# Optimization experiments

Hardware: AMD Instinct MI355X
Metric: run time of the kernel (lower is better)

## Reference

```python
import jax, jax.numpy as jnp
import numpy as np

N_OBS, N_DIM, N_FUNCTIONS, N_APPLICATIONS = 65536, 256, 16, 8


def setup_inputs() -> dict:
    key = jax.random.key(0)
    k1, k2, k3, k4 = jax.random.split(key, 4)
    x = jax.random.normal(k1, (N_OBS, N_DIM), dtype=jnp.float32)
    function_indices = jax.random.randint(k2, (N_OBS, N_APPLICATIONS), 0, N_FUNCTIONS, dtype=jnp.int32)
    # Stacked Dense weights/biases, one per IFS function. Scale keeps column
    # norms well under the MaxNorm(0.99) constraint (contractive maps).
    W = jax.random.normal(k3, (N_FUNCTIONS, N_DIM, N_DIM), dtype=jnp.float32) * 0.05
    b = jax.random.normal(k4, (N_FUNCTIONS, N_DIM), dtype=jnp.float32) * 0.05
    return {"x": x, "function_indices": function_indices, "W": W, "b": b}


def reference(x, function_indices, W, b):
    # One IFS application step: compute all n_functions affine maps for every
    # point (as the original layer does), then select the per-point function.
    def step(carry, idx):
        # carry: (n_obs, n_dim); idx: (n_obs,) int
        y_all = jnp.einsum('od,fde->ofe', carry, W) + b  # (n_obs, n_funcs, n_dim)
        y = jnp.take_along_axis(y_all, idx[:, None, None].astype(jnp.int32), axis=1)[:, 0, :]
        return y, None
    # scan over the n_applications axis (leading axis after transpose)
    out, _ = jax.lax.scan(step, x, function_indices.T)
    return out
```

## Files before the change

kernel.cpp:

```cpp
#include <hip/hip_runtime.h>
#include <hip/hip_bf16.h>
#include <stdint.h>

#define N_OBS 65536
#define N_DIM 256
#define N_FUN 16
#define N_APP 8
#define MT 64
#define PERM_STRIDE (N_OBS + N_FUN * MT)
#define MAX_TILES (PERM_STRIDE / MT)
#define N_BLK 256

typedef __attribute__((ext_vector_type(8))) short v8s;
typedef __attribute__((ext_vector_type(4))) short v4s;
typedef __attribute__((ext_vector_type(4))) float v4f;

__device__ __forceinline__ unsigned short f2bf(float f) {
  union { float f; uint32_t u; } v;
  v.f = f;
  uint32_t u = v.u;
  return (unsigned short)((u + 0x7FFFu + ((u >> 16) & 1u)) >> 16);
}

__global__ void k_init(int* __restrict__ perm) {
  int tid = blockIdx.x * 256 + threadIdx.x;
  if (tid < N_APP * PERM_STRIDE) perm[tid] = -1;
}

__global__ void k_prep_w(const float* __restrict__ W, unsigned short* __restrict__ Wt) {
  int tid = blockIdx.x * 256 + threadIdx.x;
  int f = tid >> 16;
  int n = (tid >> 8) & 255;
  int k = tid & 255;
  Wt[tid] = f2bf(W[(f << 16) | (k << 8) | n]);
}

__global__ void k_hist2(const int* __restrict__ fidx, int* __restrict__ blockCnt) {
  __shared__ int h[N_APP * N_FUN];
  int tid = threadIdx.x;
  if (tid < N_APP * N_FUN) h[tid] = 0;
  __syncthreads();
  int o = blockIdx.x * 256 + tid;
  const int4* p = (const int4*)(fidx + o * N_APP);
  int4 a = p[0], b = p[1];
  atomicAdd(&h[0 * N_FUN + a.x], 1);
  atomicAdd(&h[1 * N_FUN + a.y], 1);
  atomicAdd(&h[2 * N_FUN + a.z], 1);
  atomicAdd(&h[3 * N_FUN + a.w], 1);
  atomicAdd(&h[4 * N_FUN + b.x], 1);
  atomicAdd(&h[5 * N_FUN + b.y], 1);
  atomicAdd(&h[6 * N_FUN + b.z], 1);
  atomicAdd(&h[7 * N_FUN + b.w], 1);
  __syncthreads();
  if (tid < N_APP * N_FUN) blockCnt[tid * N_BLK + blockIdx.x] = h[tid];
}

__global__ void k_scan2(const int* __restrict__ blockCnt, int* __restrict__ pb,
                        int* __restrict__ tilef, int* __restrict__ blockOff) {
  __shared__ int tot[N_APP * N_FUN];
  int i = threadIdx.x;
  if (i < N_APP * N_FUN) {
    int s = 0;
    for (int b = 0; b < N_BLK; ++b) s += blockCnt[i * N_BLK + b];
    tot[i] = s;
  }
  __syncthreads();
  if (i < N_APP) {
    int base = 0;
    for (int f = 0; f < N_FUN; ++f) {
      pb[i * 17 + f] = base;
      int c = tot[i * N_FUN + f];
      int padded = (c + MT - 1) & ~(MT - 1);
      int q0 = base / MT, q1 = (base + padded) / MT;
      for (int q = q0; q < q1; ++q) tilef[i * MAX_TILES + q] = f;
      base += padded;
    }
    pb[i * 17 + 16] = base;
  }
  __syncthreads();
  if (i < N_APP * N_FUN) {
    int t = i >> 4, f = i & 15;
    int off = pb[t * 17 + f];
    for (int b = 0; b < N_BLK; ++b) {
      blockOff[i * N_BLK + b] = off;
      off += blockCnt[i * N_BLK + b];
    }
  }
}

__global__ void k_scatter2(const int* __restrict__ fidx, const int* __restrict__ blockOff,
                           int* __restrict__ perm) {
  __shared__ int cur[N_APP * N_FUN];
  int tid = threadIdx.x;
  if (tid < N_APP * N_FUN) cur[tid] = blockOff[tid * N_BLK + blockIdx.x];
  __syncthreads();
  int o = blockIdx.x * 256 + tid;
  const int4* p = (const int4*)(fidx + o * N_APP);
  int4 a = p[0], b = p[1];
  int fs[8] = {a.x, a.y, a.z, a.w, b.x, b.y, b.z, b.w};
  #pragma unroll
  for (int t = 0; t < N_APP; ++t) {
    int pos = atomicAdd(&cur[t * N_FUN + fs[t]], 1);
    perm[t * PERM_STRIDE + pos] = o;
  }
}

__global__ void k_pos(const int* __restrict__ perm, int* __restrict__ pos) {
  int tid = blockIdx.x * 256 + threadIdx.x;
  if (tid >= 7 * PERM_STRIDE) return;
  int t = tid / PERM_STRIDE + 1;
  int s = tid - (t - 1) * PERM_STRIDE;
  int o = perm[t * PERM_STRIDE + s];
  if (o >= 0) pos[(t - 1) * N_OBS + o] = s;
}

__global__ void k_outpos(int* __restrict__ perm, const int* __restrict__ pos,
                         int* __restrict__ outpos0) {
  int tid = blockIdx.x * 256 + threadIdx.x;
  if (tid >= 7 * PERM_STRIDE) return;
  int t = tid / PERM_STRIDE;
  int s = tid - t * PERM_STRIDE;
  int o = perm[t * PERM_STRIDE + s];
  int val = (o >= 0) ? pos[t * N_OBS + o] : -1;
  if (t == 0) outpos0[s] = val;
  else perm[t * PERM_STRIDE + s] = val;
}

template <int SRC_F32, int DST_F32>
__global__ __launch_bounds__(256, 4)
void k_step(const void* __restrict__ src_, void* __restrict__ dst_,
            const unsigned short* __restrict__ Wt, const float* __restrict__ bias,
            const int* __restrict__ pb_t, const int* __restrict__ tilef_t,
            const int* __restrict__ outpos_t, const int* __restrict__ perm0) {
  __shared__ unsigned short As[MT * N_DIM];
  __shared__ int ops[MT];
  int tile = blockIdx.x;
  if (tile * MT >= pb_t[16]) return;
  int f = tilef_t[tile];
  int tid = threadIdx.x;

  if (tid < MT) ops[tid] = outpos_t[tile * MT + tid];

  if (SRC_F32) {
    const int* permBase = perm0 + tile * MT;
    #pragma unroll
    for (int i = 0; i < 8; ++i) {
      int g = tid + i * 256;
      int row = g >> 5, c = g & 31;
      int grow = permBase[row];
      if (grow < 0) grow = 0;
      const v4f* s = (const v4f*)((const float*)src_ + ((size_t)grow << 8) + (c << 3));
      v4f v0 = s[0], v1 = s[1];
      v8s val;
      val[0] = (short)f2bf(v0[0]); val[1] = (short)f2bf(v0[1]);
      val[2] = (short)f2bf(v0[2]); val[3] = (short)f2bf(v0[3]);
      val[4] = (short)f2bf(v1[0]); val[5] = (short)f2bf(v1[1]);
      val[6] = (short)f2bf(v1[2]); val[7] = (short)f2bf(v1[3]);
      *(v8s*)((char*)As + (row << 9) + ((c ^ (row & 7)) << 4)) = val;
    }
  } else {
    const unsigned short* srcT = (const unsigned short*)src_ + (size_t)tile * MT * N_DIM;
    #pragma unroll
    for (int i = 0; i < 8; ++i) {
      int g = tid + i * 256;
      int row = g >> 5, c = g & 31;
      v8s val = *(const v8s*)(srcT + (size_t)g * 8);
      *(v8s*)((char*)As + (row << 9) + ((c ^ (row & 7)) << 4)) = val;
    }
  }
  __syncthreads();

  int lane = tid & 63, wave = tid >> 6;
  int l15 = lane & 15, lq = lane >> 4;
  v4f acc[4][4] = {};
  const unsigned short* Wf = Wt + ((size_t)f << 16);

  #pragma unroll
  for (int kk = 0; kk < 8; ++kk) {
    v8s a[4];
    #pragma unroll
    for (int mt = 0; mt < 4; ++mt) {
      int row = mt * 16 + l15;
      int byte = (row << 9) + ((((kk << 2) + lq) ^ (row & 7)) << 4);
      a[mt] = *(const v8s*)((const char*)As + byte);
    }
    #pragma unroll
    for (int nt = 0; nt < 4; ++nt) {
      int n = wave * 64 + nt * 16 + l15;
      v8s bfr = *(const v8s*)(Wf + n * N_DIM + (kk << 5) + (lq << 3));
      #pragma unroll
      for (int mt = 0; mt < 4; ++mt)
        acc[mt][nt] = __builtin_amdgcn_mfma_f32_16x16x32_bf16(bfr, a[mt], acc[mt][nt], 0, 0, 0);
    }
  }

  const float* bf_ = bias + f * N_DIM;
  if (DST_F32) {
    float* dout = (float*)dst_;
    #pragma unroll
    for (int mt = 0; mt < 4; ++mt) {
      int m = mt * 16 + l15;
      int orow = ops[m];
      if (orow >= 0) {
        #pragma unroll
        for (int nt = 0; nt < 4; ++nt) {
          int n0 = wave * 64 + nt * 16 + lq * 4;
          v4f bv = *(const v4f*)(bf_ + n0);
          v4f o = acc[mt][nt] + bv;
          *(v4f*)(dout + ((size_t)orow << 8) + n0) = o;
        }
      }
    }
  } else {
    __syncthreads();
    #pragma unroll
    for (int mt = 0; mt < 4; ++mt) {
      int m = mt * 16 + l15;
      #pragma unroll
      for (int nt = 0; nt < 4; ++nt) {
        int n0 = wave * 64 + nt * 16 + lq * 4;
        v4f bv = *(const v4f*)(bf_ + n0);
        v4s pk;
        pk[0] = (short)f2bf(acc[mt][nt][0] + bv[0]);
        pk[1] = (short)f2bf(acc[mt][nt][1] + bv[1]);
        pk[2] = (short)f2bf(acc[mt][nt][2] + bv[2]);
        pk[3] = (short)f2bf(acc[mt][nt][3] + bv[3]);
        int c = n0 >> 3;
        *(v4s*)((char*)As + (m << 9) + ((c ^ (m & 7)) << 4) + ((n0 & 7) << 1)) = pk;
      }
    }
    __syncthreads();
    unsigned short* dst = (unsigned short*)dst_;
    #pragma unroll
    for (int i = 0; i < 8; ++i) {
      int g = tid + i * 256;
      int row = g >> 5, c = g & 31;
      int op = ops[row];
      if (op >= 0) {
        v8s v = *(const v8s*)((char*)As + (row << 9) + ((c ^ (row & 7)) << 4));
        *(v8s*)(dst + (size_t)op * N_DIM + c * 8) = v;
      }
    }
  }
}

extern "C" void kernel_launch(void* const* d_in, const int* in_sizes, int n_in,
                              void* d_out, int out_size, void* d_ws, size_t ws_size,
                              hipStream_t stream) {
  const float* x = (const float*)d_in[0];
  const int* fidx = (const int*)d_in[1];
  const float* W = (const float*)d_in[2];
  const float* bias = (const float*)d_in[3];

  char* ws = (char*)d_ws;
  unsigned short* carryA = (unsigned short*)ws;
  int* blockCnt = (int*)ws;
  int* blockOff = (int*)(ws + 131072);
  int* pos      = (int*)(ws + 262144);
  unsigned short* Wt = (unsigned short*)(ws + 34078720);
  int* perm    = (int*)(ws + 36175872);
  int* pb      = (int*)(ws + 38305792);
  int* tilef   = (int*)(ws + 38306336);
  int* outpos0 = (int*)(ws + 38339648);
  unsigned short* carryB = (unsigned short*)d_out;

  k_init<<<(N_APP * PERM_STRIDE + 255) / 256, 256, 0, stream>>>(perm);
  k_prep_w<<<(N_FUN * N_DIM * N_DIM) / 256, 256, 0, stream>>>(W, Wt);
  k_hist2<<<N_BLK, 256, 0, stream>>>(fidx, blockCnt);
  k_scan2<<<1, 128, 0, stream>>>(blockCnt, pb, tilef, blockOff);
  k_scatter2<<<N_BLK, 256, 0, stream>>>(fidx, blockOff, perm);
  k_pos<<<(7 * PERM_STRIDE + 255) / 256, 256, 0, stream>>>(perm, pos);
  k_outpos<<<(7 * PERM_STRIDE + 255) / 256, 256, 0, stream>>>(perm, pos, outpos0);

  k_step<1, 0><<<MAX_TILES, 256, 0, stream>>>(x, carryA, Wt, bias, pb, tilef, outpos0, perm);
  for (int t = 1; t < 7; ++t) {
    const unsigned short* s = (t & 1) ? carryA : carryB;
    unsigned short* d = (t & 1) ? carryB : carryA;
    k_step<0, 0><<<MAX_TILES, 256, 0, stream>>>(
        s, d, Wt, bias, pb + t * 17, tilef + t * MAX_TILES,
        perm + t * PERM_STRIDE, nullptr);
  }
  k_step<0, 1><<<MAX_TILES, 256, 0, stream>>>(
      carryA, d_out, Wt, bias, pb + 7 * 17, tilef + 7 * MAX_TILES,
      perm + 7 * PERM_STRIDE, nullptr);
}
```

Measured before the change: 388.1 us.

## Compose pairs of affine maps to halve the number of sequential GEMM steps

When the workspace is large enough, the code precomputes all 256 composed matrices W_f·W_g and the matching composed biases. Each point is then bucketed by its pair of consecutive function indices, so the forward pass runs 4 grouped GEMM steps instead of 8. This removes half of the per-step activation reads and writes and the launch overhead, at the cost of an extra composition GEMM and more padded tiles, since there are 256 groups instead of 16. Rounding the composed matrices to bf16 changes numerics. It also adds an XCD-aware block swizzle and raises the occupancy hint to 5.

```diff
diff --git a/kernel.cpp b/kernel.cpp
--- a/kernel.cpp
+++ b/kernel.cpp
@@ -7,8 +7,6 @@
 #define N_FUN 16
 #define N_APP 8
 #define MT 64
-#define PERM_STRIDE (N_OBS + N_FUN * MT)
-#define MAX_TILES (PERM_STRIDE / MT)
 #define N_BLK 256
 
 typedef __attribute__((ext_vector_type(8))) short v8s;
@@ -22,65 +20,73 @@
   return (unsigned short)((u + 0x7FFFu + ((u >> 16) & 1u)) >> 16);
 }
 
-__global__ void k_init(int* __restrict__ perm) {
+__device__ __forceinline__ int xcd_swz(int bid, int n) {
+  int q = n >> 3;
+  return (bid & 7) * q + (bid >> 3);
+}
+
+__global__ void k_init(int* __restrict__ perm, int total) {
   int tid = blockIdx.x * 256 + threadIdx.x;
-  if (tid < N_APP * PERM_STRIDE) perm[tid] = -1;
+  if (tid < total) perm[tid] = -1;
 }
 
 __global__ void k_prep_w(const float* __restrict__ W, unsigned short* __restrict__ Wt) {
   int tid = blockIdx.x * 256 + threadIdx.x;
-  int f = tid >> 16;
-  int n = (tid >> 8) & 255;
-  int k = tid & 255;
+  int f = tid >> 16, n = (tid >> 8) & 255, k = tid & 255;
   Wt[tid] = f2bf(W[(f << 16) | (k << 8) | n]);
 }
 
-__global__ void k_hist2(const int* __restrict__ fidx, int* __restrict__ blockCnt) {
-  __shared__ int h[N_APP * N_FUN];
+__global__ void k_hist(const int* __restrict__ fidx, int* __restrict__ blockCnt,
+                       int pairMode) {
+  __shared__ int h[1024];
+  int nb = pairMode ? 1024 : 128;
   int tid = threadIdx.x;
-  if (tid < N_APP * N_FUN) h[tid] = 0;
-  __syncthreads();
-  int o = blockIdx.x * 256 + tid;
-  const int4* p = (const int4*)(fidx + o * N_APP);
+  for (int j = tid; j < nb; j += 256) h[j] = 0;
+  __syncthreads();
+  size_t o = blockIdx.x * 256 + tid;
+  const int4* p = (const int4*)(fidx + o * 8);
   int4 a = p[0], b = p[1];
-  atomicAdd(&h[0 * N_FUN + a.x], 1);
-  atomicAdd(&h[1 * N_FUN + a.y], 1);
-  atomicAdd(&h[2 * N_FUN + a.z], 1);
-  atomicAdd(&h[3 * N_FUN + a.w], 1);
-  atomicAdd(&h[4 * N_FUN + b.x], 1);
-  atomicAdd(&h[5 * N_FUN + b.y], 1);
-  atomicAdd(&h[6 * N_FUN + b.z], 1);
-  atomicAdd(&h[7 * N_FUN + b.w], 1);
-  __syncthreads();
-  if (tid < N_APP * N_FUN) blockCnt[tid * N_BLK + blockIdx.x] = h[tid];
-}
-
-__global__ void k_scan2(const int* __restrict__ blockCnt, int* __restrict__ pb,
-                        int* __restrict__ tilef, int* __restrict__ blockOff) {
-  __shared__ int tot[N_APP * N_FUN];
+  int fs[8] = {a.x, a.y, a.z, a.w, b.x, b.y, b.z, b.w};
+  if (pairMode) {
+    #pragma unroll
+    for (int t = 0; t < 4; ++t)
+      atomicAdd(&h[t * 256 + fs[2 * t] * 16 + fs[2 * t + 1]], 1);
+  } else {
+    #pragma unroll
+    for (int t = 0; t < 8; ++t) atomicAdd(&h[t * 16 + fs[t]], 1);
+  }
+  __syncthreads();
+  for (int j = tid; j < nb; j += 256) blockCnt[j * N_BLK + blockIdx.x] = h[j];
+}
+
+__global__ void k_scan(const int* __restrict__ blockCnt, int* __restrict__ pb,
+                       int* __restrict__ tilef, int* __restrict__ blockOff,
+                       int ns, int ng, int maxt) {
+  __shared__ int tot[1024];
   int i = threadIdx.x;
-  if (i < N_APP * N_FUN) {
+  int nb = ns * ng;
+  if (i < nb) {
     int s = 0;
     for (int b = 0; b < N_BLK; ++b) s += blockCnt[i * N_BLK + b];
     tot[i] = s;
   }
   __syncthreads();
-  if (i < N_APP) {
+  if (i < ns) {
     int base = 0;
-    for (int f = 0; f < N_FUN; ++f) {
-      pb[i * 17 + f] = base;
-      int c = tot[i * N_FUN + f];
+    for (int f = 0; f < ng; ++f) {
+      pb[i * (ng + 1) + f] = base;
+      int c = tot[i * ng + f];
       int padded = (c + MT - 1) & ~(MT - 1);
-      int q0 = base / MT, q1 = (base + padded) / MT;
-      for (int q = q0; q < q1; ++q) tilef[i * MAX_TILES + q] = f;
+      int q1 = (base + padded) >> 6;
+      for (int q = base >> 6; q < q1; ++q) tilef[i * maxt + q] = f;
       base += padded;
     }
-    pb[i * 17 + 16] = base;
-  }
-  __syncthreads();
-  if (i < N_APP * N_FUN) {
-    int t = i >> 4, f = i & 15;
-    int off = pb[t * 17 + f];
+    pb[i * (ng + 1) + ng] = base;
+  }
+  __syncthreads();
+  if (i < nb) {
+    int t = i / ng, f = i - t * ng;
+    int off = pb[t * (ng + 1) + f];
     for (int b = 0; b < N_BLK; ++b) {
       blockOff[i * N_BLK + b] = off;
       off += blockCnt[i * N_BLK + b];
@@ -88,65 +94,148 @@
   }
 }
 
-__global__ void k_scatter2(const int* __restrict__ fidx, const int* __restrict__ blockOff,
-                           int* __restrict__ perm) {
-  __shared__ int cur[N_APP * N_FUN];
+__global__ void k_scatter(const int* __restrict__ fidx, const int* __restrict__ blockOff,
+                          int* __restrict__ perm, int pairMode, int stride) {
+  __shared__ int cur[1024];
+  int nb = pairMode ? 1024 : 128;
   int tid = threadIdx.x;
-  if (tid < N_APP * N_FUN) cur[tid] = blockOff[tid * N_BLK + blockIdx.x];
-  __syncthreads();
-  int o = blockIdx.x * 256 + tid;
-  const int4* p = (const int4*)(fidx + o * N_APP);
+  for (int j = tid; j < nb; j += 256) cur[j] = blockOff[j * N_BLK + blockIdx.x];
+  __syncthreads();
+  size_t o = blockIdx.x * 256 + tid;
+  const int4* p = (const int4*)(fidx + o * 8);
   int4 a = p[0], b = p[1];
   int fs[8] = {a.x, a.y, a.z, a.w, b.x, b.y, b.z, b.w};
-  #pragma unroll
-  for (int t = 0; t < N_APP; ++t) {
-    int pos = atomicAdd(&cur[t * N_FUN + fs[t]], 1);
-    perm[t * PERM_STRIDE + pos] = o;
-  }
-}
-
-__global__ void k_pos(const int* __restrict__ perm, int* __restrict__ pos) {
+  if (pairMode) {
+    #pragma unroll
+    for (int t = 0; t < 4; ++t) {
+      int pos = atomicAdd(&cur[t * 256 + fs[2 * t] * 16 + fs[2 * t + 1]], 1);
+      perm[t * stride + pos] = (int)o;
+    }
+  } else {
+    #pragma unroll
+    for (int t = 0; t < 8; ++t) {
+      int pos = atomicAdd(&cur[t * 16 + fs[t]], 1);
+      perm[t * stride + pos] = (int)o;
+    }
+  }
+}
+
+__global__ void k_pos(const int* __restrict__ perm, int* __restrict__ pos,
+                      int stride, int total) {
   int tid = blockIdx.x * 256 + threadIdx.x;
-  if (tid >= 7 * PERM_STRIDE) return;
-  int t = tid / PERM_STRIDE + 1;
-  int s = tid - (t - 1) * PERM_STRIDE;
-  int o = perm[t * PERM_STRIDE + s];
+  if (tid >= total) return;
+  int t = tid / stride + 1, s = tid - (t - 1) * stride;
+  int o = perm[t * stride + s];
   if (o >= 0) pos[(t - 1) * N_OBS + o] = s;
 }
 
 __global__ void k_outpos(int* __restrict__ perm, const int* __restrict__ pos,
-                         int* __restrict__ outpos0) {
+                         int* __restrict__ outpos0, int stride, int total) {
   int tid = blockIdx.x * 256 + threadIdx.x;
-  if (tid >= 7 * PERM_STRIDE) return;
-  int t = tid / PERM_STRIDE;
-  int s = tid - t * PERM_STRIDE;
-  int o = perm[t * PERM_STRIDE + s];
+  if (tid >= total) return;
+  int t = tid / stride, s = tid - t * stride;
+  int o = perm[t * stride + s];
   int val = (o >= 0) ? pos[t * N_OBS + o] : -1;
   if (t == 0) outpos0[s] = val;
-  else perm[t * PERM_STRIDE + s] = val;
+  else perm[t * stride + s] = val;
+}
+
+__global__ void k_biasc(const float* __restrict__ W, const float* __restrict__ b,
+                        float* __restrict__ bc) {
+  int pair = blockIdx.x, e = threadIdx.x;
+  int f = pair >> 4, g = pair & 15;
+  const float* Wg = W + ((size_t)g << 16);
+  const float* bf_ = b + (f << 8);
+  float acc = b[(g << 8) + e];
+  for (int k = 0; k < 256; ++k) acc += bf_[k] * Wg[(k << 8) + e];
+  bc[(pair << 8) + e] = acc;
+}
+
+__global__ __launch_bounds__(256, 5)
+void k_compose(const float* __restrict__ W, const unsigned short* __restrict__ Wt,
+               unsigned short* __restrict__ Wc) {
+  __shared__ unsigned short As[MT * N_DIM];
+  int bid = xcd_swz(blockIdx.x, gridDim.x);
+  int pair = bid >> 2, dt = bid & 3;
+  int f = pair >> 4, g = pair & 15;
+  int tid = threadIdx.x;
+  #pragma unroll
+  for (int i = 0; i < 8; ++i) {
+    int g0 = tid + i * 256;
+    int row = g0 >> 5, c = g0 & 31;
+    const v4f* s = (const v4f*)(W + ((size_t)f << 16) + ((dt * 64 + row) << 8) + (c << 3));
+    v4f v0 = s[0], v1 = s[1];
+    v8s val;
+    val[0] = (short)f2bf(v0[0]); val[1] = (short)f2bf(v0[1]);
+    val[2] = (short)f2bf(v0[2]); val[3] = (short)f2bf(v0[3]);
+    val[4] = (short)f2bf(v1[0]); val[5] = (short)f2bf(v1[1]);
+    val[6] = (short)f2bf(v1[2]); val[7] = (short)f2bf(v1[3]);
+    *(v8s*)((char*)As + (row << 9) + ((c ^ (row & 7)) << 4)) = val;
+  }
+  __syncthreads();
+  int lane = tid & 63, wave = tid >> 6, l15 = lane & 15, lq = lane >> 4;
+  v4f acc[4][4] = {};
+  const unsigned short* Wg = Wt + ((size_t)g << 16);
+  #pragma unroll
+  for (int kk = 0; kk < 8; ++kk) {
+    v8s a[4];
+    #pragma unroll
+    for (int mt = 0; mt < 4; ++mt) {
+      int row = mt * 16 + l15;
+      a[mt] = *(const v8s*)((const char*)As + (row << 9) + ((((kk << 2) + lq) ^ (row & 7)) << 4));
+    }
+    #pragma unroll
+    for (int nt = 0; nt < 4; ++nt) {
+      int n = wave * 64 + nt * 16 + l15;
+      v8s bfr = *(const v8s*)(Wg + n * N_DIM + (kk << 5) + (lq << 3));
+      #pragma unroll
+      for (int mt = 0; mt < 4; ++mt)
+        acc[mt][nt] = __builtin_amdgcn_mfma_f32_16x16x32_bf16(a[mt], bfr, acc[mt][nt], 0, 0, 0);
+    }
+  }
+  __syncthreads();
+  #pragma unroll
+  for (int mt = 0; mt < 4; ++mt) {
+    #pragma unroll
+    for (int nt = 0; nt < 4; ++nt) {
+      int e = wave * 64 + nt * 16 + l15;
+      int m0 = mt * 16 + lq * 4;
+      v4s pk;
+      pk[0] = (short)f2bf(acc[mt][nt][0]);
+      pk[1] = (short)f2bf(acc[mt][nt][1]);
+      pk[2] = (short)f2bf(acc[mt][nt][2]);
+      pk[3] = (short)f2bf(acc[mt][nt][3]);
+      *(v4s*)((char*)As + (e << 7) + ((m0 << 1) ^ ((e & 7) << 4))) = pk;
+    }
+  }
+  __syncthreads();
+  #pragma unroll
+  for (int i = 0; i < 8; ++i) {
+    int g0 = tid + i * 256;
+    int e = g0 >> 3, c = g0 & 7;
+    v8s v = *(const v8s*)((char*)As + (e << 7) + (((c << 4) ^ ((e & 7) << 4))));
+    *(v8s*)(Wc + ((size_t)pair << 16) + (e << 8) + (dt << 6) + (c << 3)) = v;
+  }
 }
 
 template <int SRC_F32, int DST_F32>
-__global__ __launch_bounds__(256, 4)
+__global__ __launch_bounds__(256, 5)
 void k_step(const void* __restrict__ src_, void* __restrict__ dst_,
-            const unsigned short* __restrict__ Wt, const float* __restrict__ bias,
+            const unsigned short* __restrict__ Wmat, const float* __restrict__ bias,
             const int* __restrict__ pb_t, const int* __restrict__ tilef_t,
-            const int* __restrict__ outpos_t, const int* __restrict__ perm0) {
+            const int* __restrict__ outpos_t, const int* __restrict__ perm0, int ng) {
   __shared__ unsigned short As[MT * N_DIM];
-  __shared__ int ops[MT];
-  int tile = blockIdx.x;
-  if (tile * MT >= pb_t[16]) return;
+  int tile = xcd_swz(blockIdx.x, gridDim.x);
+  if (tile * MT >= pb_t[ng]) return;
   int f = tilef_t[tile];
   int tid = threadIdx.x;
 
-  if (tid < MT) ops[tid] = outpos_t[tile * MT + tid];
-
   if (SRC_F32) {
     const int* permBase = perm0 + tile * MT;
     #pragma unroll
     for (int i = 0; i < 8; ++i) {
-      int g = tid + i * 256;
-      int row = g >> 5, c = g & 31;
+      int g0 = tid + i * 256;
+      int row = g0 >> 5, c = g0 & 31;
       int grow = permBase[row];
       if (grow < 0) grow = 0;
       const v4f* s = (const v4f*)((const float*)src_ + ((size_t)grow << 8) + (c << 3));
@@ -162,18 +251,17 @@
     const unsigned short* srcT = (const unsigned short*)src_ + (size_t)tile * MT * N_DIM;
     #pragma unroll
     for (int i = 0; i < 8; ++i) {
-      int g = tid + i * 256;
-      int row = g >> 5, c = g & 31;
-      v8s val = *(const v8s*)(srcT + (size_t)g * 8);
+      int g0 = tid + i * 256;
+      int row = g0 >> 5, c = g0 & 31;
+      v8s val = *(const v8s*)(srcT + (size_t)g0 * 8);
       *(v8s*)((char*)As + (row << 9) + ((c ^ (row & 7)) << 4)) = val;
     }
   }
   __syncthreads();
 
-  int lane = tid & 63, wave = tid >> 6;
-  int l15 = lane & 15, lq = lane >> 4;
+  int lane = tid & 63, wave = tid >> 6, l15 = lane & 15, lq = lane >> 4;
   v4f acc[4][4] = {};
-  const unsigned short* Wf = Wt + ((size_t)f << 16);
+  const unsigned short* Wf = Wmat + ((size_t)f << 16);
 
   #pragma unroll
   for (int kk = 0; kk < 8; ++kk) {
@@ -181,8 +269,7 @@
     #pragma unroll
     for (int mt = 0; mt < 4; ++mt) {
       int row = mt * 16 + l15;
-      int byte = (row << 9) + ((((kk << 2) + lq) ^ (row & 7)) << 4);
-      a[mt] = *(const v8s*)((const char*)As + byte);
+      a[mt] = *(const v8s*)((const char*)As + (row << 9) + ((((kk << 2) + lq) ^ (row & 7)) << 4));
     }
     #pragma unroll
     for (int nt = 0; nt < 4; ++nt) {
@@ -200,7 +287,7 @@
     #pragma unroll
     for (int mt = 0; mt < 4; ++mt) {
       int m = mt * 16 + l15;
-      int orow = ops[m];
+      int orow = outpos_t[tile * MT + m];
       if (orow >= 0) {
         #pragma unroll
         for (int nt = 0; nt < 4; ++nt) {
@@ -226,16 +313,16 @@
         pk[2] = (short)f2bf(acc[mt][nt][2] + bv[2]);
         pk[3] = (short)f2bf(acc[mt][nt][3] + bv[3]);
         int c = n0 >> 3;
-        *(v4s*)((char*)As + (m << 9) + ((c ^ (m & 7)) << 4) + ((n0 & 7) << 1)) = pk;
+        *(v4s*)((char*)As + (m << 9) + (((c ^ (m & 7)) << 4)) + ((n0 & 7) << 1)) = pk;
       }
     }
     __syncthreads();
     unsigned short* dst = (unsigned short*)dst_;
     #pragma unroll
     for (int i = 0; i < 8; ++i) {
-      int g = tid + i * 256;
-      int row = g >> 5, c = g & 31;
-      int op = ops[row];
+      int g0 = tid + i * 256;
+      int row = g0 >> 5, c = g0 & 31;
+      int op = outpos_t[tile * MT + row];
       if (op >= 0) {
         v8s v = *(const v8s*)((char*)As + (row << 9) + ((c ^ (row & 7)) << 4));
         *(v8s*)(dst + (size_t)op * N_DIM + c * 8) = v;
@@ -251,36 +338,70 @@
   const int* fidx = (const int*)d_in[1];
   const float* W = (const float*)d_in[2];
   const float* bias = (const float*)d_in[3];
-
   char* ws = (char*)d_ws;
-  unsigned short* carryA = (unsigned short*)ws;
-  int* blockCnt = (int*)ws;
-  int* blockOff = (int*)(ws + 131072);
-  int* pos      = (int*)(ws + 262144);
-  unsigned short* Wt = (unsigned short*)(ws + 34078720);
-  int* perm    = (int*)(ws + 36175872);
-  int* pb      = (int*)(ws + 38305792);
-  int* tilef   = (int*)(ws + 38306336);
-  int* outpos0 = (int*)(ws + 38339648);
-  unsigned short* carryB = (unsigned short*)d_out;
-
-  k_init<<<(N_APP * PERM_STRIDE + 255) / 256, 256, 0, stream>>>(perm);
-  k_prep_w<<<(N_FUN * N_DIM * N_DIM) / 256, 256, 0, stream>>>(W, Wt);
-  k_hist2<<<N_BLK, 256, 0, stream>>>(fidx, blockCnt);
-  k_scan2<<<1, 128, 0, stream>>>(blockCnt, pb, tilef, blockOff);
-  k_scatter2<<<N_BLK, 256, 0, stream>>>(fidx, blockOff, perm);
-  k_pos<<<(7 * PERM_STRIDE + 255) / 256, 256, 0, stream>>>(perm, pos);
-  k_outpos<<<(7 * PERM_STRIDE + 255) / 256, 256, 0, stream>>>(perm, pos, outpos0);
-
-  k_step<1, 0><<<MAX_TILES, 256, 0, stream>>>(x, carryA, Wt, bias, pb, tilef, outpos0, perm);
-  for (int t = 1; t < 7; ++t) {
-    const unsigned short* s = (t & 1) ? carryA : carryB;
-    unsigned short* d = (t & 1) ? carryB : carryA;
-    k_step<0, 0><<<MAX_TILES, 256, 0, stream>>>(
-        s, d, Wt, bias, pb + t * 17, tilef + t * MAX_TILES,
-        perm + t * PERM_STRIDE, nullptr);
-  }
-  k_step<0, 1><<<MAX_TILES, 256, 0, stream>>>(
-      carryA, d_out, Wt, bias, pb + 7 * 17, tilef + 7 * MAX_TILES,
-      perm + 7 * PERM_STRIDE, nullptr);
-}
+
+  const size_t NEED_PAIR = 80u * 1024u * 1024u;
+  if (ws_size >= NEED_PAIR) {
+    const int NS = 4, NG = 256, STRIDE = 81920, MAXT = 1280;
+    unsigned short* carryA = (unsigned short*)ws;
+    int* blockCnt = (int*)ws;
+    int* blockOff = (int*)(ws + 1048576);
+    int* pos      = (int*)(ws + 2097152);
+    unsigned short* Wc = (unsigned short*)(ws + 41943040);
+    unsigned short* Wt = (unsigned short*)(ws + 75497472);
+    float* bc    = (float*)(ws + 77594624);
+    int* perm    = (int*)(ws + 77856768);
+    int* pb      = (int*)(ws + 79167488);
+    int* tilef   = (int*)(ws + 79171600);
+    int* outpos0 = (int*)(ws + 79192080);
+    unsigned short* carryB = (unsigned short*)d_out;
+
+    k_init<<<(NS * STRIDE + 255) / 256, 256, 0, stream>>>(perm, NS * STRIDE);
+    k_prep_w<<<(N_FUN * 65536) / 256, 256, 0, stream>>>(W, Wt);
+    k_hist<<<N_BLK, 256, 0, stream>>>(fidx, blockCnt, 1);
+    k_scan<<<1, 1024, 0, stream>>>(blockCnt, pb, tilef, blockOff, NS, NG, MAXT);
+    k_scatter<<<N_BLK, 256, 0, stream>>>(fidx, blockOff, perm, 1, STRIDE);
+    k_pos<<<((NS - 1) * STRIDE + 255) / 256, 256, 0, stream>>>(perm, pos, STRIDE, (NS - 1) * STRIDE);
+    k_outpos<<<((NS - 1) * STRIDE + 255) / 256, 256, 0, stream>>>(perm, pos, outpos0, STRIDE, (NS - 1) * STRIDE);
+    k_biasc<<<256, 256, 0, stream>>>(W, bias, bc);
+    k_compose<<<1024, 256, 0, stream>>>(W, Wt, Wc);
+
+    k_step<1, 0><<<MAXT, 256, 0, stream>>>(x, carryA, Wc, bc, pb, tilef, outpos0, perm, NG);
+    k_step<0, 0><<<MAXT, 256, 0, stream>>>(carryA, carryB, Wc, bc,
+        pb + 1 * (NG + 1), tilef + 1 * MAXT, perm + 1 * STRIDE, nullptr, NG);
+    k_step<0, 0><<<MAXT, 256, 0, stream>>>(carryB, carryA, Wc, bc,
+        pb + 2 * (NG + 1), tilef + 2 * MAXT, perm + 2 * STRIDE, nullptr, NG);
+    k_step<0, 1><<<MAXT, 256, 0, stream>>>(carryA, d_out, Wc, bc,
+        pb + 3 * (NG + 1), tilef + 3 * MAXT, perm + 3 * STRIDE, nullptr, NG);
+  } else {
+    const int NS = 8, NG = 16, STRIDE = 66560, MAXT = 1040;
+    unsigned short* carryA = (unsigned short*)ws;
+    int* blockCnt = (int*)ws;
+    int* blockOff = (int*)(ws + 1048576);
+    int* pos      = (int*)(ws + 2097152);
+    unsigned short* Wt = (unsigned short*)(ws + 34078720);
+    int* perm    = (int*)(ws + 36175872);
+    int* pb      = (int*)(ws + 38305792);
+    int* tilef   = (int*)(ws + 38306336);
+    int* outpos0 = (int*)(ws + 38339616);
+    unsigned short* carryB = (unsigned short*)d_out;
+
+    k_init<<<(NS * STRIDE + 255) / 256, 256, 0, stream>>>(perm, NS * STRIDE);
+    k_prep_w<<<(N_FUN * 65536) / 256, 256, 0, stream>>>(W, Wt);
+    k_hist<<<N_BLK, 256, 0, stream>>>(fidx, blockCnt, 0);
+    k_scan<<<1, 1024, 0, stream>>>(blockCnt, pb, tilef, blockOff, NS, NG, MAXT);
+    k_scatter<<<N_BLK, 256, 0, stream>>>(fidx, blockOff, perm, 0, STRIDE);
+    k_pos<<<((NS - 1) * STRIDE + 255) / 256, 256, 0, stream>>>(perm, pos, STRIDE, (NS - 1) * STRIDE);
+    k_outpos<<<((NS - 1) * STRIDE + 255) / 256, 256, 0, stream>>>(perm, pos, outpos0, STRIDE, (NS - 1) * STRIDE);
+
+    k_step<1, 0><<<MAXT, 256, 0, stream>>>(x, carryA, Wt, bias, pb, tilef, outpos0, perm, NG);
+    for (int t = 1; t < NS - 1; ++t) {
+      const unsigned short* s = (t & 1) ? carryA : carryB;
+      unsigned short* d = (t & 1) ? carryB : carryA;
+      k_step<0, 0><<<MAXT, 256, 0, stream>>>(s, d, Wt, bias,
+          pb + t * (NG + 1), tilef + t * MAXT, perm + t * STRIDE, nullptr, NG);
+    }
+    k_step<0, 1><<<MAXT, 256, 0, stream>>>(carryA, d_out, Wt, bias,
+        pb + (NS - 1) * (NG + 1), tilef + (NS - 1) * MAXT, perm + (NS - 1) * STRIDE, nullptr, NG);
+  }
+}
```

Result: slower. 606.1 us (+56.2%).

## Drop LDS staging in step GEMM; per-wave 16-row tiles with XCD swizzle

Applied to the files above, without the earlier changes.

The step kernel no longer stages a 64-row tile in shared memory. Each wave loads its 16 rows of A directly into registers and computes half of the output columns, and blocks are remapped so that consecutive tiles land on the same XCD. The single-thread scan is split into parallel reduction, base and prefix-scan kernels. This removes LDS traffic and barriers and adds parallelism to preprocessing, but each wave now reads W from global memory with less reuse per row.

```diff
diff --git a/kernel.cpp b/kernel.cpp
--- a/kernel.cpp
+++ b/kernel.cpp
@@ -7,8 +7,8 @@
 #define N_FUN 16
 #define N_APP 8
 #define MT 64
-#define PERM_STRIDE (N_OBS + N_FUN * MT)
-#define MAX_TILES (PERM_STRIDE / MT)
+#define STRIDE 66560
+#define MAXT 1040
 #define N_BLK 256
 
 typedef __attribute__((ext_vector_type(8))) short v8s;
@@ -22,26 +22,29 @@
   return (unsigned short)((u + 0x7FFFu + ((u >> 16) & 1u)) >> 16);
 }
 
-__global__ void k_init(int* __restrict__ perm) {
-  int tid = blockIdx.x * 256 + threadIdx.x;
-  if (tid < N_APP * PERM_STRIDE) perm[tid] = -1;
+__device__ __forceinline__ int xcd_swz(int bid, int n) {
+  int q = n >> 3;
+  return (bid & 7) * q + (bid >> 3);
+}
+
+__global__ void k_init(int* __restrict__ perm, int total) {
+  int tid = blockIdx.x * 256 + threadIdx.x;
+  if (tid < total) perm[tid] = -1;
 }
 
 __global__ void k_prep_w(const float* __restrict__ W, unsigned short* __restrict__ Wt) {
   int tid = blockIdx.x * 256 + threadIdx.x;
-  int f = tid >> 16;
-  int n = (tid >> 8) & 255;
-  int k = tid & 255;
+  int f = tid >> 16, n = (tid >> 8) & 255, k = tid & 255;
   Wt[tid] = f2bf(W[(f << 16) | (k << 8) | n]);
 }
 
-__global__ void k_hist2(const int* __restrict__ fidx, int* __restrict__ blockCnt) {
+__global__ void k_hist(const int* __restrict__ fidx, int* __restrict__ blockCnt) {
   __shared__ int h[N_APP * N_FUN];
   int tid = threadIdx.x;
   if (tid < N_APP * N_FUN) h[tid] = 0;
   __syncthreads();
-  int o = blockIdx.x * 256 + tid;
-  const int4* p = (const int4*)(fidx + o * N_APP);
+  size_t o = blockIdx.x * 256 + tid;
+  const int4* p = (const int4*)(fidx + o * 8);
   int4 a = p[0], b = p[1];
   atomicAdd(&h[0 * N_FUN + a.x], 1);
   atomicAdd(&h[1 * N_FUN + a.y], 1);
@@ -55,75 +58,95 @@
   if (tid < N_APP * N_FUN) blockCnt[tid * N_BLK + blockIdx.x] = h[tid];
 }
 
-__global__ void k_scan2(const int* __restrict__ blockCnt, int* __restrict__ pb,
-                        int* __restrict__ tilef, int* __restrict__ blockOff) {
-  __shared__ int tot[N_APP * N_FUN];
-  int i = threadIdx.x;
-  if (i < N_APP * N_FUN) {
-    int s = 0;
-    for (int b = 0; b < N_BLK; ++b) s += blockCnt[i * N_BLK + b];
-    tot[i] = s;
-  }
-  __syncthreads();
-  if (i < N_APP) {
+__global__ void k_tot(const int* __restrict__ blockCnt, int* __restrict__ tot) {
+  __shared__ int s[256];
+  int tid = threadIdx.x;
+  s[tid] = blockCnt[blockIdx.x * N_BLK + tid];
+  __syncthreads();
+  for (int o = 128; o > 0; o >>= 1) {
+    if (tid < o) s[tid] += s[tid + o];
+    __syncthreads();
+  }
+  if (tid == 0) tot[blockIdx.x] = s[0];
+}
+
+__global__ void k_base(const int* __restrict__ tot, int* __restrict__ pb,
+                       int* __restrict__ tilef) {
+  __shared__ int pbl[N_APP * 17];
+  int tid = threadIdx.x;
+  if (tid < N_APP) {
     int base = 0;
     for (int f = 0; f < N_FUN; ++f) {
-      pb[i * 17 + f] = base;
-      int c = tot[i * N_FUN + f];
-      int padded = (c + MT - 1) & ~(MT - 1);
-      int q0 = base / MT, q1 = (base + padded) / MT;
-      for (int q = q0; q < q1; ++q) tilef[i * MAX_TILES + q] = f;
-      base += padded;
-    }
-    pb[i * 17 + 16] = base;
-  }
-  __syncthreads();
-  if (i < N_APP * N_FUN) {
-    int t = i >> 4, f = i & 15;
-    int off = pb[t * 17 + f];
-    for (int b = 0; b < N_BLK; ++b) {
-      blockOff[i * N_BLK + b] = off;
-      off += blockCnt[i * N_BLK + b];
-    }
-  }
-}
-
-__global__ void k_scatter2(const int* __restrict__ fidx, const int* __restrict__ blockOff,
-                           int* __restrict__ perm) {
+      pbl[tid * 17 + f] = base;
+      int c = tot[tid * N_FUN + f];
+      base += (c + MT - 1) & ~(MT - 1);
+    }
+    pbl[tid * 17 + 16] = base;
+  }
+  __syncthreads();
+  if (tid < N_APP * 17) pb[tid] = pbl[tid];
+  for (int idx = tid; idx < N_APP * MAXT; idx += 256) {
+    int t = idx / MAXT, q = idx - t * MAXT;
+    int posn = q * MT;
+    int fg = 0;
+    #pragma unroll
+    for (int f = 1; f < N_FUN; ++f)
+      if (posn >= pbl[t * 17 + f]) fg = f;
+    tilef[idx] = fg;
+  }
+}
+
+__global__ void k_off(const int* __restrict__ blockCnt, const int* __restrict__ pb,
+                      int* __restrict__ blockOff) {
+  __shared__ int s[256];
+  int bin = blockIdx.x, tid = threadIdx.x;
+  int c = blockCnt[bin * N_BLK + tid];
+  s[tid] = c;
+  __syncthreads();
+  for (int o = 1; o < 256; o <<= 1) {
+    int v = (tid >= o) ? s[tid - o] : 0;
+    __syncthreads();
+    s[tid] += v;
+    __syncthreads();
+  }
+  int t = bin >> 4, f = bin & 15;
+  blockOff[bin * N_BLK + tid] = pb[t * 17 + f] + s[tid] - c;
+}
+
+__global__ void k_scatter(const int* __restrict__ fidx, const int* __restrict__ blockOff,
+                          int* __restrict__ perm) {
   __shared__ int cur[N_APP * N_FUN];
   int tid = threadIdx.x;
   if (tid < N_APP * N_FUN) cur[tid] = blockOff[tid * N_BLK + blockIdx.x];
   __syncthreads();
-  int o = blockIdx.x * 256 + tid;
-  const int4* p = (const int4*)(fidx + o * N_APP);
+  size_t o = blockIdx.x * 256 + tid;
+  const int4* p = (const int4*)(fidx + o * 8);
   int4 a = p[0], b = p[1];
   int fs[8] = {a.x, a.y, a.z, a.w, b.x, b.y, b.z, b.w};
   #pragma unroll
   for (int t = 0; t < N_APP; ++t) {
     int pos = atomicAdd(&cur[t * N_FUN + fs[t]], 1);
-    perm[t * PERM_STRIDE + pos] = o;
+    perm[t * STRIDE + pos] = (int)o;
   }
 }
 
 __global__ void k_pos(const int* __restrict__ perm, int* __restrict__ pos) {
   int tid = blockIdx.x * 256 + threadIdx.x;
-  if (tid >= 7 * PERM_STRIDE) return;
-  int t = tid / PERM_STRIDE + 1;
-  int s = tid - (t - 1) * PERM_STRIDE;
-  int o = perm[t * PERM_STRIDE + s];
+  if (tid >= 7 * STRIDE) return;
+  int t = tid / STRIDE + 1, s = tid - (t - 1) * STRIDE;
+  int o = perm[t * STRIDE + s];
   if (o >= 0) pos[(t - 1) * N_OBS + o] = s;
 }
 
 __global__ void k_outpos(int* __restrict__ perm, const int* __restrict__ pos,
                          int* __restrict__ outpos0) {
   int tid = blockIdx.x * 256 + threadIdx.x;
-  if (tid >= 7 * PERM_STRIDE) return;
-  int t = tid / PERM_STRIDE;
-  int s = tid - t * PERM_STRIDE;
-  int o = perm[t * PERM_STRIDE + s];
+  if (tid >= 7 * STRIDE) return;
+  int t = tid / STRIDE, s = tid - t * STRIDE;
+  int o = perm[t * STRIDE + s];
   int val = (o >= 0) ? pos[t * N_OBS + o] : -1;
   if (t == 0) outpos0[s] = val;
-  else perm[t * PERM_STRIDE + s] = val;
+  else perm[t * STRIDE + s] = val;
 }
 
 template <int SRC_F32, int DST_F32>
@@ -132,114 +155,73 @@
             const unsigned short* __restrict__ Wt, const float* __restrict__ bias,
             const int* __restrict__ pb_t, const int* __restrict__ tilef_t,
             const int* __restrict__ outpos_t, const int* __restrict__ perm0) {
-  __shared__ unsigned short As[MT * N_DIM];
-  __shared__ int ops[MT];
-  int tile = blockIdx.x;
-  if (tile * MT >= pb_t[16]) return;
+  int tid = threadIdx.x;
+  int bid = xcd_swz(blockIdx.x, gridDim.x);
+  int gw = bid * 4 + (tid >> 6);
+  int rg = gw >> 1, half = gw & 1;
+  if (rg * 16 >= pb_t[16]) return;
+  int lane = tid & 63, l15 = lane & 15, lq = lane >> 4;
+  int tile = rg >> 2;
   int f = tilef_t[tile];
-  int tid = threadIdx.x;
-
-  if (tid < MT) ops[tid] = outpos_t[tile * MT + tid];
-
+  int myrow = rg * 16 + l15;
+
+  v8s a[8];
   if (SRC_F32) {
-    const int* permBase = perm0 + tile * MT;
-    #pragma unroll
-    for (int i = 0; i < 8; ++i) {
-      int g = tid + i * 256;
-      int row = g >> 5, c = g & 31;
-      int grow = permBase[row];
-      if (grow < 0) grow = 0;
-      const v4f* s = (const v4f*)((const float*)src_ + ((size_t)grow << 8) + (c << 3));
-      v4f v0 = s[0], v1 = s[1];
-      v8s val;
-      val[0] = (short)f2bf(v0[0]); val[1] = (short)f2bf(v0[1]);
-      val[2] = (short)f2bf(v0[2]); val[3] = (short)f2bf(v0[3]);
-      val[4] = (short)f2bf(v1[0]); val[5] = (short)f2bf(v1[1]);
-      val[6] = (short)f2bf(v1[2]); val[7] = (short)f2bf(v1[3]);
-      *(v8s*)((char*)As + (row << 9) + ((c ^ (row & 7)) << 4)) = val;
+    int grow = perm0[myrow];
+    if (grow < 0) grow = 0;
+    const float* xr = (const float*)src_ + ((size_t)grow << 8) + (lq << 3);
+    #pragma unroll
+    for (int kk = 0; kk < 8; ++kk) {
+      v4f v0 = *(const v4f*)(xr + kk * 32);
+      v4f v1 = *(const v4f*)(xr + kk * 32 + 4);
+      v8s t;
+      t[0] = (short)f2bf(v0[0]); t[1] = (short)f2bf(v0[1]);
+      t[2] = (short)f2bf(v0[2]); t[3] = (short)f2bf(v0[3]);
+      t[4] = (short)f2bf(v1[0]); t[5] = (short)f2bf(v1[1]);
+      t[6] = (short)f2bf(v1[2]); t[7] = (short)f2bf(v1[3]);
+      a[kk] = t;
     }
   } else {
-    const unsigned short* srcT = (const unsigned short*)src_ + (size_t)tile * MT * N_DIM;
-    #pragma unroll
-    for (int i = 0; i < 8; ++i) {
-      int g = tid + i * 256;
-      int row = g >> 5, c = g & 31;
-      v8s val = *(const v8s*)(srcT + (size_t)g * 8);
-      *(v8s*)((char*)As + (row << 9) + ((c ^ (row & 7)) << 4)) = val;
-    }
-  }
-  __syncthreads();
-
-  int lane = tid & 63, wave = tid >> 6;
-  int l15 = lane & 15, lq = lane >> 4;
-  v4f acc[4][4] = {};
-  const unsigned short* Wf = Wt + ((size_t)f << 16);
-
+    const unsigned short* sr = (const unsigned short*)src_ + ((size_t)myrow << 8) + (lq << 3);
+    #pragma unroll
+    for (int kk = 0; kk < 8; ++kk)
+      a[kk] = *(const v8s*)(sr + kk * 32);
+  }
+
+  v4f acc[8] = {};
+  const unsigned short* Wf =
+      Wt + ((size_t)f << 16) + ((size_t)((half << 7) + l15) << 8) + (lq << 3);
   #pragma unroll
   for (int kk = 0; kk < 8; ++kk) {
-    v8s a[4];
-    #pragma unroll
-    for (int mt = 0; mt < 4; ++mt) {
-      int row = mt * 16 + l15;
-      int byte = (row << 9) + ((((kk << 2) + lq) ^ (row & 7)) << 4);
-      a[mt] = *(const v8s*)((const char*)As + byte);
-    }
-    #pragma unroll
-    for (int nt = 0; nt < 4; ++nt) {
-      int n = wave * 64 + nt * 16 + l15;
-      v8s bfr = *(const v8s*)(Wf + n * N_DIM + (kk << 5) + (lq << 3));
-      #pragma unroll
-      for (int mt = 0; mt < 4; ++mt)
-        acc[mt][nt] = __builtin_amdgcn_mfma_f32_16x16x32_bf16(bfr, a[mt], acc[mt][nt], 0, 0, 0);
-    }
-  }
-
-  const float* bf_ = bias + f * N_DIM;
+    #pragma unroll
+    for (int nt = 0; nt < 8; ++nt) {
+      v8s bfr = *(const v8s*)(Wf + (nt << 12) + (kk << 5));
+      acc[nt] = __builtin_amdgcn_mfma_f32_16x16x32_bf16(bfr, a[kk], acc[nt], 0, 0, 0);
+    }
+  }
+
+  int op = outpos_t[myrow];
+  if (op < 0) return;
+  const float* bf_ = bias + (f << 8) + (half << 7) + (lq << 2);
   if (DST_F32) {
-    float* dout = (float*)dst_;
-    #pragma unroll
-    for (int mt = 0; mt < 4; ++mt) {
-      int m = mt * 16 + l15;
-      int orow = ops[m];
-      if (orow >= 0) {
-        #pragma unroll
-        for (int nt = 0; nt < 4; ++nt) {
-          int n0 = wave * 64 + nt * 16 + lq * 4;
-          v4f bv = *(const v4f*)(bf_ + n0);
-          v4f o = acc[mt][nt] + bv;
-          *(v4f*)(dout + ((size_t)orow << 8) + n0) = o;
-        }
-      }
+    float* dr = (float*)dst_ + ((size_t)op << 8) + (half << 7) + (lq << 2);
+    #pragma unroll
+    for (int nt = 0; nt < 8; ++nt) {
+      v4f bv = *(const v4f*)(bf_ + (nt << 4));
+      v4f o = acc[nt] + bv;
+      *(v4f*)(dr + (nt << 4)) = o;
     }
   } else {
-    __syncthreads();
-    #pragma unroll
-    for (int mt = 0; mt < 4; ++mt) {
-      int m = mt * 16 + l15;
-      #pragma unroll
-      for (int nt = 0; nt < 4; ++nt) {
-        int n0 = wave * 64 + nt * 16 + lq * 4;
-        v4f bv = *(const v4f*)(bf_ + n0);
-        v4s pk;
-        pk[0] = (short)f2bf(acc[mt][nt][0] + bv[0]);
-        pk[1] = (short)f2bf(acc[mt][nt][1] + bv[1]);
-        pk[2] = (short)f2bf(acc[mt][nt][2] + bv[2]);
-        pk[3] = (short)f2bf(acc[mt][nt][3] + bv[3]);
-        int c = n0 >> 3;
-        *(v4s*)((char*)As + (m << 9) + ((c ^ (m & 7)) << 4) + ((n0 & 7) << 1)) = pk;
-      }
-    }
-    __syncthreads();
-    unsigned short* dst = (unsigned short*)dst_;
-    #pragma unroll
-    for (int i = 0; i < 8; ++i) {
-      int g = tid + i * 256;
-      int row = g >> 5, c = g & 31;
-      int op = ops[row];
-      if (op >= 0) {
-        v8s v = *(const v8s*)((char*)As + (row << 9) + ((c ^ (row & 7)) << 4));
-        *(v8s*)(dst + (size_t)op * N_DIM + c * 8) = v;
-      }
+    unsigned short* dr = (unsigned short*)dst_ + ((size_t)op << 8) + (half << 7) + (lq << 2);
+    #pragma unroll
+    for (int nt = 0; nt < 8; ++nt) {
+      v4f bv = *(const v4f*)(bf_ + (nt << 4));
+      v4s pk;
+      pk[0] = (short)f2bf(acc[nt][0] + bv[0]);
+      pk[1] = (short)f2bf(acc[nt][1] + bv[1]);
+      pk[2] = (short)f2bf(acc[nt][2] + bv[2]);
+      pk[3] = (short)f2bf(acc[nt][3] + bv[3]);
+      *(v4s*)(dr + (nt << 4)) = pk;
     }
   }
 }
@@ -251,36 +233,38 @@
   const int* fidx = (const int*)d_in[1];
   const float* W = (const float*)d_in[2];
   const float* bias = (const float*)d_in[3];
-
   char* ws = (char*)d_ws;
+
   unsigned short* carryA = (unsigned short*)ws;
   int* blockCnt = (int*)ws;
   int* blockOff = (int*)(ws + 131072);
-  int* pos      = (int*)(ws + 262144);
+  int* tot      = (int*)(ws + 262144);
+  int* pos      = (int*)(ws + 262656);
   unsigned short* Wt = (unsigned short*)(ws + 34078720);
   int* perm    = (int*)(ws + 36175872);
   int* pb      = (int*)(ws + 38305792);
   int* tilef   = (int*)(ws + 38306336);
-  int* outpos0 = (int*)(ws + 38339648);
+  int* outpos0 = (int*)(ws + 38339616);
   unsigned short* carryB = (unsigned short*)d_out;
 
-  k_init<<<(N_APP * PERM_STRIDE + 255) / 256, 256, 0, stream>>>(perm);
-  k_prep_w<<<(N_FUN * N_DIM * N_DIM) / 256, 256, 0, stream>>>(W, Wt);
-  k_hist2<<<N_BLK, 256, 0, stream>>>(fidx, blockCnt);
-  k_scan2<<<1, 128, 0, stream>>>(blockCnt, pb, tilef, blockOff);
-  k_scatter2<<<N_BLK, 256, 0, stream>>>(fidx, blockOff, perm);
-  k_pos<<<(7 * PERM_STRIDE + 255) / 256, 256, 0, stream>>>(perm, pos);
-  k_outpos<<<(7 * PERM_STRIDE + 255) / 256, 256, 0, stream>>>(perm, pos, outpos0);
-
-  k_step<1, 0><<<MAX_TILES, 256, 0, stream>>>(x, carryA, Wt, bias, pb, tilef, outpos0, perm);
+  k_init<<<(N_APP * STRIDE + 255) / 256, 256, 0, stream>>>(perm, N_APP * STRIDE);
+  k_prep_w<<<(N_FUN * 65536) / 256, 256, 0, stream>>>(W, Wt);
+  k_hist<<<N_BLK, 256, 0, stream>>>(fidx, blockCnt);
+  k_tot<<<128, 256, 0, stream>>>(blockCnt, tot);
+  k_base<<<1, 256, 0, stream>>>(tot, pb, tilef);
+  k_off<<<128, 256, 0, stream>>>(blockCnt, pb, blockOff);
+  k_scatter<<<N_BLK, 256, 0, stream>>>(fidx, blockOff, perm);
+  k_pos<<<(7 * STRIDE + 255) / 256, 256, 0, stream>>>(perm, pos);
+  k_outpos<<<(7 * STRIDE + 255) / 256, 256, 0, stream>>>(perm, pos, outpos0);
+
+  const int GS = 2080;
+  k_step<1, 0><<<GS, 256, 0, stream>>>(x, carryA, Wt, bias, pb, tilef, outpos0, perm);
   for (int t = 1; t < 7; ++t) {
     const unsigned short* s = (t & 1) ? carryA : carryB;
     unsigned short* d = (t & 1) ? carryB : carryA;
-    k_step<0, 0><<<MAX_TILES, 256, 0, stream>>>(
-        s, d, Wt, bias, pb + t * 17, tilef + t * MAX_TILES,
-        perm + t * PERM_STRIDE, nullptr);
-  }
-  k_step<0, 1><<<MAX_TILES, 256, 0, stream>>>(
-      carryA, d_out, Wt, bias, pb + 7 * 17, tilef + 7 * MAX_TILES,
-      perm + 7 * PERM_STRIDE, nullptr);
-}
+    k_step<0, 0><<<GS, 256, 0, stream>>>(
+        s, d, Wt, bias, pb + t * 17, tilef + t * MAXT, perm + t * STRIDE, nullptr);
+  }
+  k_step<0, 1><<<GS, 256, 0, stream>>>(
+      carryA, d_out, Wt, bias, pb + 7 * 17, tilef + 7 * MAXT, perm + 7 * STRIDE, nullptr);
+}
```

Result: slower. 705.5 us (+81.8%).
